# Kernel tuning notes

Measured on AMD Instinct MI355X. Metric: run time of the kernel, lower is better.

The kernel has to match this reference:

```python
import jax, jax.numpy as jnp
import numpy as np
from jax import lax

NUM_VARS = 16384
NUM_CHECKS = 8192
BATCH = 32
MAX_ITER = 15
H_DENSITY = 0.001  # ~8 ones per column, LDPC-like Tanner graph


def setup_inputs() -> dict:
    key = jax.random.key(0)
    k_h, k_s, k_l = jax.random.split(key, 3)
    # Sparse binary parity-check matrix represented densely (same math).
    parity_matrix = (jax.random.uniform(k_h, (NUM_CHECKS, NUM_VARS)) < H_DENSITY).astype(jnp.float32)
    syndrome = jax.random.randint(k_s, (BATCH, NUM_CHECKS), 0, 2).astype(jnp.float32)
    channel_llrs = jax.random.normal(k_l, (BATCH, NUM_VARS), dtype=jnp.float32)
    w_vc = jnp.ones((1,), dtype=jnp.float32)
    w_cv = jnp.ones((1,), dtype=jnp.float32)
    damping = jnp.float32(0.5)
    return {
        "syndrome": syndrome,
        "parity_matrix": parity_matrix,
        "channel_llrs": channel_llrs,
        "w_vc": w_vc,
        "w_cv": w_cv,
        "damping": damping,
    }


def reference(syndrome, parity_matrix, channel_llrs, w_vc, w_cv, damping):
    # syndrome: (B, C); parity_matrix H: (C, V); channel_llrs: (B, V)
    s_sign = 1.0 - 2.0 * syndrome  # (B, C)

    def body(v_beliefs, _):
        # v -> c: sparse.mm(H, v^T)^T == v @ H^T  -> (B, C)
        v_to_c = w_vc * (v_beliefs @ parity_matrix.T)
        c_msg = s_sign * jnp.tanh(v_to_c * 0.5)  # (B, C)
        # c -> v: sparse.mm(H^T, c^T)^T == c @ H  -> (B, V)
        c_to_v = w_cv * (c_msg @ parity_matrix)
        v_new = damping * v_beliefs + (1.0 - damping) * (channel_llrs + c_to_v)
        return v_new, None

    v_beliefs, _ = lax.scan(body, channel_llrs, None, length=MAX_ITER)
    return jax.nn.sigmoid(-v_beliefs)  # (B, V) bit-flip probabilities
```

## Files before the change

### kernel.cpp

```cpp
#include <hip/hip_runtime.h>


#define C_NUM 8192
#define V_NUM 16384
#define B_NUM 32
#define RW 64
#define CW 32

#define NBLK 256
#define NTHR 1024
#define NTH (NBLK * NTHR)

#define WCAP 256

typedef unsigned short u16;
typedef unsigned int u32;
typedef unsigned long long u64;

#define ZERO_WORDS ((C_NUM * 4 + V_NUM * 4 + C_NUM * RW * 2 + V_NUM * CW * 2) / 4)
#define NBAR 31
#define BAR_STRIDE 64

__device__ __forceinline__ float agent_ldf(const float* p) {
    return __hip_atomic_load(p, __ATOMIC_RELAXED, __HIP_MEMORY_SCOPE_AGENT);
}
__device__ __forceinline__ void agent_stf(float* p, float v) {
    __hip_atomic_store(p, v, __ATOMIC_RELAXED, __HIP_MEMORY_SCOPE_AGENT);
}
__device__ __forceinline__ u64 agent_ld64(const u64* p) {
    return __hip_atomic_load(p, __ATOMIC_RELAXED, __HIP_MEMORY_SCOPE_AGENT);
}
__device__ __forceinline__ int agent_ldi(const int* p) {
    return __hip_atomic_load(p, __ATOMIC_RELAXED, __HIP_MEMORY_SCOPE_AGENT);
}
__device__ __forceinline__ void agent_st32(u32* p, u32 v) {
    __hip_atomic_store(p, v, __ATOMIC_RELAXED, __HIP_MEMORY_SCOPE_AGENT);
}
__device__ __forceinline__ void agent_st16(u16* p, u16 v) {
    __hip_atomic_store(p, v, __ATOMIC_RELAXED, __HIP_MEMORY_SCOPE_AGENT);
}

__device__ __forceinline__ void grid_barrier(u32* bars, int id) {
    __syncthreads();
    if (threadIdx.x == 0) {
        u32* base = bars + id * 8 * BAR_STRIDE;
        asm volatile("s_waitcnt vmcnt(0) lgkmcnt(0)" ::: "memory");
        __hip_atomic_fetch_add(base + (blockIdx.x & 7) * BAR_STRIDE, 1u,
                               __ATOMIC_RELAXED, __HIP_MEMORY_SCOPE_AGENT);
        u32 sum;
        do {
            sum = 0;
#pragma unroll
            for (int g = 0; g < 8; ++g)
                sum += __hip_atomic_load(base + g * BAR_STRIDE,
                                         __ATOMIC_RELAXED, __HIP_MEMORY_SCOPE_AGENT);
            if (sum < (u32)NBLK) __builtin_amdgcn_s_sleep(4);
        } while (sum < (u32)NBLK);
        asm volatile("" ::: "memory");
    }
    __syncthreads();
}

__device__ __forceinline__ float fast_tanh_half(float x) {
    float ax = fabsf(x);
    float e = __expf(-ax);
    return copysignf((1.0f - e) / (1.0f + e), x);
}

__global__ __launch_bounds__(NTHR, 1)
void bp_fused(const float* __restrict__ H,
              const float* __restrict__ synd,
              const float* __restrict__ llr,
              const float* __restrict__ w_vc_p,
              const float* __restrict__ w_cv_p,
              const float* __restrict__ damp_p,
              int* __restrict__ row_cnt, int* __restrict__ col_cnt,
              u16* __restrict__ row_idx, u16* __restrict__ col_idx,
              float* __restrict__ bel, float* __restrict__ cms,
              u32* __restrict__ bars,
              float* __restrict__ out) {
    const int tid = blockIdx.x * NTHR + threadIdx.x;
    const int lane = threadIdx.x & 63;

    __shared__ u32 lds_edges[(NTHR / 64) * WCAP];
    u32* const wl = lds_edges + (threadIdx.x >> 6) * WCAP;

    {
        u32* zp = (u32*)row_cnt;
        for (int t = tid; t < ZERO_WORDS; t += NTH) agent_st32(&zp[t], 0u);
    }
    float llr_r[2], bel_r[2];
#pragma unroll
    for (int r = 0; r < 2; ++r) {
        int i = tid + r * NTH;
        int b = i & 31, v = i >> 5;
        float x = llr[b * V_NUM + v];
        llr_r[r] = x; bel_r[r] = x;
        agent_stf(&bel[i], x);
    }
    float ss_r;
    {
        int b = tid & 31, c = tid >> 5;
        ss_r = 1.0f - 2.0f * synd[b * C_NUM + c];
    }

    int wave_cnt;
    {
        const float4* Hv = (const float4*)H;
        const u64 ltmask = (1ull << lane) - 1ull;
        int wb = 0;
#pragma unroll 2
        for (int itn = 0; itn < 64; ++itn) {
            int t = tid + itn * (2 * NTH);
            float4 h0 = Hv[t];
            float4 h1 = Hv[t + NTH];
            float vals[8] = {h0.x, h0.y, h0.z, h0.w, h1.x, h1.y, h1.z, h1.w};
#pragma unroll
            for (int k = 0; k < 8; ++k) {
                bool nz = vals[k] != 0.0f;
                u64 b = __ballot(nz);
                if (b) {
                    if (nz) {
                        int ee = (k < 4) ? (t * 4 + k)
                                         : ((t + NTH) * 4 + (k - 4));
                        int off = wb + (int)__popcll(b & ltmask);
                        if (off < WCAP) wl[off] = (u32)ee;
                    }
                    wb += (int)__popcll(b);
                }
            }
        }
        wave_cnt = wb < WCAP ? wb : WCAP;
    }
    grid_barrier(bars, 0);

    {
        for (int e = lane; e < wave_cnt; e += 64) {
            u32 ee = wl[e];
            int c = (int)(ee >> 14);
            int v = (int)(ee & (V_NUM - 1));
            int rs = atomicAdd(&row_cnt[c], 1);
            if (rs < RW) agent_st16(&row_idx[c * RW + rs], (u16)v);
            int cs = atomicAdd(&col_cnt[v], 1);
            if (cs < CW) agent_st16(&col_idx[v * CW + cs], (u16)c);
        }
    }
    grid_barrier(bars, 1);

    int nrow_r;
    {
        int n = agent_ldi(&row_cnt[tid >> 5]);
        nrow_r = n > RW ? RW : n;
    }
    int ncol_r[2];
#pragma unroll
    for (int r = 0; r < 2; ++r) {
        int n = agent_ldi(&col_cnt[(tid + r * NTH) >> 5]);
        ncol_r[r] = n > CW ? CW : n;
    }
    const float wvc = w_vc_p[0];
    const float wcv = w_cv_p[0];
    const float d   = damp_p[0];

    int barid = 2;
    for (int it = 0; it < 15; ++it) {
        {
            int b = tid & 31, c = tid >> 5;
            int n = nrow_r;
            const u64* q4 = (const u64*)(row_idx + c * RW);
            float sum = 0.0f;
            int k4 = (n + 3) >> 2;
            for (int p = 0; p < k4; ++p) {
                u64 q = agent_ld64(&q4[p]);
                int j = 4 * p;
                int i0 = (int)(q & 0xFFFFu);
                int i1 = (int)((q >> 16) & 0xFFFFu);
                int i2 = (int)((q >> 32) & 0xFFFFu);
                int i3 = (int)(q >> 48);
                float s0 = agent_ldf(&bel[i0 * B_NUM + b]);
                float s1 = agent_ldf(&bel[i1 * B_NUM + b]);
                float s2 = agent_ldf(&bel[i2 * B_NUM + b]);
                float s3 = agent_ldf(&bel[i3 * B_NUM + b]);
                sum += s0;
                sum += (j + 1 < n) ? s1 : 0.0f;
                sum += (j + 2 < n) ? s2 : 0.0f;
                sum += (j + 3 < n) ? s3 : 0.0f;
            }
            agent_stf(&cms[tid], ss_r * fast_tanh_half(wvc * sum));
        }
        grid_barrier(bars, barid++);

        bool last = (it == 14);
#pragma unroll
        for (int r = 0; r < 2; ++r) {
            int i = tid + r * NTH;
            int b = i & 31, v = i >> 5;
            int n = ncol_r[r];
            const u64* q4 = (const u64*)(col_idx + v * CW);
            float sum = 0.0f;
            int k4 = (n + 3) >> 2;
            for (int p = 0; p < k4; ++p) {
                u64 q = agent_ld64(&q4[p]);
                int j = 4 * p;
                int i0 = (int)(q & 0xFFFFu);
                int i1 = (int)((q >> 16) & 0xFFFFu);
                int i2 = (int)((q >> 32) & 0xFFFFu);
                int i3 = (int)(q >> 48);
                float s0 = agent_ldf(&cms[i0 * B_NUM + b]);
                float s1 = agent_ldf(&cms[i1 * B_NUM + b]);
                float s2 = agent_ldf(&cms[i2 * B_NUM + b]);
                float s3 = agent_ldf(&cms[i3 * B_NUM + b]);
                sum += s0;
                sum += (j + 1 < n) ? s1 : 0.0f;
                sum += (j + 2 < n) ? s2 : 0.0f;
                sum += (j + 3 < n) ? s3 : 0.0f;
            }
            float nb = d * bel_r[r] + (1.0f - d) * (llr_r[r] + wcv * sum);
            bel_r[r] = nb;
            if (!last) {
                agent_stf(&bel[i], nb);
            } else {
                out[b * V_NUM + v] = 1.0f / (1.0f + __expf(nb));
            }
        }
        if (!last) grid_barrier(bars, barid++);
    }
}

extern "C" void kernel_launch(void* const* d_in, const int* in_sizes, int n_in,
                              void* d_out, int out_size, void* d_ws, size_t ws_size,
                              hipStream_t stream) {
    const float* synd = (const float*)d_in[0];
    const float* H    = (const float*)d_in[1];
    const float* llr  = (const float*)d_in[2];
    const float* w_vc = (const float*)d_in[3];
    const float* w_cv = (const float*)d_in[4];
    const float* damp = (const float*)d_in[5];
    float* out = (float*)d_out;

    char* ws = (char*)d_ws;
    size_t off = 0;
    int* row_cnt = (int*)(ws + off); off += (size_t)C_NUM * 4;
    int* col_cnt = (int*)(ws + off); off += (size_t)V_NUM * 4;
    u16* row_idx = (u16*)(ws + off); off += (size_t)C_NUM * RW * 2;
    u16* col_idx = (u16*)(ws + off); off += (size_t)V_NUM * CW * 2;
    float* bel = (float*)(ws + off); off += (size_t)V_NUM * B_NUM * 4;
    float* cms = (float*)(ws + off); off += (size_t)C_NUM * B_NUM * 4;
    u32* bars  = (u32*)(ws + off); off += (size_t)NBAR * 8 * BAR_STRIDE * 4;

    hipMemsetAsync(bars, 0, (size_t)NBAR * 8 * BAR_STRIDE * 4, stream);

    void* args[] = {
        (void*)&H, (void*)&synd, (void*)&llr,
        (void*)&w_vc, (void*)&w_cv, (void*)&damp,
        (void*)&row_cnt, (void*)&col_cnt, (void*)&row_idx, (void*)&col_idx,
        (void*)&bel, (void*)&cms, (void*)&bars, (void*)&out
    };
    hipLaunchCooperativeKernel((const void*)bp_fused,
                               dim3(NBLK), dim3(NTHR), args, 0, stream);
}
```

Before: 980.7 us.

## Cache row/column adjacency in registers, pad with zero sentinels, prefetch H scan

Before the iteration loop, each thread loads its check-node and variable-node neighbour index lists into registers (up to 48 row and 32 column entries). Unused slots point at a zeroed sentinel belief/message entry, so the per-element bounds selects go away. This removes the repeated index loads from global memory in each of the 15 iterations. The H compaction loop gains software prefetching of the next float4 pair. Risks are higher register pressure (launch bounds changed to 4) and silent truncation of rows with more than 48 nonzeros.

```diff
diff --git a/kernel.cpp b/kernel.cpp
--- a/kernel.cpp
+++ b/kernel.cpp
@@ -6,6 +6,9 @@
 #define B_NUM 32
 #define RW 64
 #define CW 32
+
+#define RQ 12
+#define CQ 8
 
 #define NBLK 256
 #define NTHR 1024
@@ -67,7 +70,7 @@
     return copysignf((1.0f - e) / (1.0f + e), x);
 }
 
-__global__ __launch_bounds__(NTHR, 1)
+__global__ __launch_bounds__(NTHR, 4)
 void bp_fused(const float* __restrict__ H,
               const float* __restrict__ synd,
               const float* __restrict__ llr,
@@ -88,6 +91,8 @@
     {
         u32* zp = (u32*)row_cnt;
         for (int t = tid; t < ZERO_WORDS; t += NTH) agent_st32(&zp[t], 0u);
+        if (tid < 32) agent_stf(&bel[V_NUM * B_NUM + tid], 0.0f);
+        else if (tid < 64) agent_stf(&cms[C_NUM * B_NUM + (tid - 32)], 0.0f);
     }
     float llr_r[2], bel_r[2];
 #pragma unroll
@@ -109,12 +114,15 @@
         const float4* Hv = (const float4*)H;
         const u64 ltmask = (1ull << lane) - 1ull;
         int wb = 0;
-#pragma unroll 2
+        int t = tid;
+        float4 c0 = Hv[t];
+        float4 c1 = Hv[t + NTH];
+#pragma unroll 1
         for (int itn = 0; itn < 64; ++itn) {
-            int t = tid + itn * (2 * NTH);
-            float4 h0 = Hv[t];
-            float4 h1 = Hv[t + NTH];
-            float vals[8] = {h0.x, h0.y, h0.z, h0.w, h1.x, h1.y, h1.z, h1.w};
+            float4 n0, n1;
+            int tn = t + 2 * NTH;
+            if (itn < 63) { n0 = Hv[tn]; n1 = Hv[tn + NTH]; }
+            float vals[8] = {c0.x, c0.y, c0.z, c0.w, c1.x, c1.y, c1.z, c1.w};
 #pragma unroll
             for (int k = 0; k < 8; ++k) {
                 bool nz = vals[k] != 0.0f;
@@ -129,6 +137,7 @@
                     wb += (int)__popcll(b);
                 }
             }
+            c0 = n0; c1 = n1; t = tn;
         }
         wave_cnt = wb < WCAP ? wb : WCAP;
     }
@@ -148,43 +157,64 @@
     grid_barrier(bars, 1);
 
     int nrow_r;
+    u64 rq[RQ];
     {
         int n = agent_ldi(&row_cnt[tid >> 5]);
-        nrow_r = n > RW ? RW : n;
+        nrow_r = n > 4 * RQ ? 4 * RQ : n;
+        const u64* q4 = (const u64*)(row_idx + (tid >> 5) * RW);
+#pragma unroll
+        for (int p = 0; p < RQ; ++p) {
+            u64 q = agent_ld64(&q4[p]);
+            int j = 4 * p;
+            u64 a0 = (j + 0 < nrow_r) ? (q & 0xFFFFu) : (u64)V_NUM;
+            u64 a1 = (j + 1 < nrow_r) ? ((q >> 16) & 0xFFFFu) : (u64)V_NUM;
+            u64 a2 = (j + 2 < nrow_r) ? ((q >> 32) & 0xFFFFu) : (u64)V_NUM;
+            u64 a3 = (j + 3 < nrow_r) ? (q >> 48) : (u64)V_NUM;
+            rq[p] = a0 | (a1 << 16) | (a2 << 32) | (a3 << 48);
+        }
     }
     int ncol_r[2];
+    u64 cq[2][CQ];
 #pragma unroll
     for (int r = 0; r < 2; ++r) {
-        int n = agent_ldi(&col_cnt[(tid + r * NTH) >> 5]);
-        ncol_r[r] = n > CW ? CW : n;
+        int v = (tid + r * NTH) >> 5;
+        int n = agent_ldi(&col_cnt[v]);
+        ncol_r[r] = n > 4 * CQ ? 4 * CQ : n;
+        const u64* q4 = (const u64*)(col_idx + v * CW);
+#pragma unroll
+        for (int p = 0; p < CQ; ++p) {
+            u64 q = agent_ld64(&q4[p]);
+            int j = 4 * p;
+            u64 a0 = (j + 0 < ncol_r[r]) ? (q & 0xFFFFu) : (u64)C_NUM;
+            u64 a1 = (j + 1 < ncol_r[r]) ? ((q >> 16) & 0xFFFFu) : (u64)C_NUM;
+            u64 a2 = (j + 2 < ncol_r[r]) ? ((q >> 32) & 0xFFFFu) : (u64)C_NUM;
+            u64 a3 = (j + 3 < ncol_r[r]) ? (q >> 48) : (u64)C_NUM;
+            cq[r][p] = a0 | (a1 << 16) | (a2 << 32) | (a3 << 48);
+        }
     }
     const float wvc = w_vc_p[0];
     const float wcv = w_cv_p[0];
     const float d   = damp_p[0];
 
+    const int b_lo = tid & 31;
     int barid = 2;
     for (int it = 0; it < 15; ++it) {
         {
-            int b = tid & 31, c = tid >> 5;
-            int n = nrow_r;
-            const u64* q4 = (const u64*)(row_idx + c * RW);
             float sum = 0.0f;
-            int k4 = (n + 3) >> 2;
-            for (int p = 0; p < k4; ++p) {
-                u64 q = agent_ld64(&q4[p]);
-                int j = 4 * p;
-                int i0 = (int)(q & 0xFFFFu);
-                int i1 = (int)((q >> 16) & 0xFFFFu);
-                int i2 = (int)((q >> 32) & 0xFFFFu);
-                int i3 = (int)(q >> 48);
-                float s0 = agent_ldf(&bel[i0 * B_NUM + b]);
-                float s1 = agent_ldf(&bel[i1 * B_NUM + b]);
-                float s2 = agent_ldf(&bel[i2 * B_NUM + b]);
-                float s3 = agent_ldf(&bel[i3 * B_NUM + b]);
-                sum += s0;
-                sum += (j + 1 < n) ? s1 : 0.0f;
-                sum += (j + 2 < n) ? s2 : 0.0f;
-                sum += (j + 3 < n) ? s3 : 0.0f;
+#pragma unroll
+            for (int p = 0; p < RQ; ++p) {
+                if (4 * p < nrow_r) {
+                    u64 q = rq[p];
+                    int i0 = (int)(q & 0xFFFFu);
+                    int i1 = (int)((q >> 16) & 0xFFFFu);
+                    int i2 = (int)((q >> 32) & 0xFFFFu);
+                    int i3 = (int)(q >> 48);
+                    float s0 = agent_ldf(&bel[i0 * B_NUM + b_lo]);
+                    float s1 = agent_ldf(&bel[i1 * B_NUM + b_lo]);
+                    float s2 = agent_ldf(&bel[i2 * B_NUM + b_lo]);
+                    float s3 = agent_ldf(&bel[i3 * B_NUM + b_lo]);
+                    sum += s0; sum += s1; sum += s2; sum += s3;
+                }
             }
             agent_stf(&cms[tid], ss_r * fast_tanh_half(wvc * sum));
         }
@@ -193,33 +223,29 @@
         bool last = (it == 14);
 #pragma unroll
         for (int r = 0; r < 2; ++r) {
-            int i = tid + r * NTH;
-            int b = i & 31, v = i >> 5;
-            int n = ncol_r[r];
-            const u64* q4 = (const u64*)(col_idx + v * CW);
             float sum = 0.0f;
-            int k4 = (n + 3) >> 2;
-            for (int p = 0; p < k4; ++p) {
-                u64 q = agent_ld64(&q4[p]);
-                int j = 4 * p;
-                int i0 = (int)(q & 0xFFFFu);
-                int i1 = (int)((q >> 16) & 0xFFFFu);
-                int i2 = (int)((q >> 32) & 0xFFFFu);
-                int i3 = (int)(q >> 48);
-                float s0 = agent_ldf(&cms[i0 * B_NUM + b]);
-                float s1 = agent_ldf(&cms[i1 * B_NUM + b]);
-                float s2 = agent_ldf(&cms[i2 * B_NUM + b]);
-                float s3 = agent_ldf(&cms[i3 * B_NUM + b]);
-                sum += s0;
-                sum += (j + 1 < n) ? s1 : 0.0f;
-                sum += (j + 2 < n) ? s2 : 0.0f;
-                sum += (j + 3 < n) ? s3 : 0.0f;
+#pragma unroll
+            for (int p = 0; p < CQ; ++p) {
+                if (4 * p < ncol_r[r]) {
+                    u64 q = cq[r][p];
+                    int i0 = (int)(q & 0xFFFFu);
+                    int i1 = (int)((q >> 16) & 0xFFFFu);
+                    int i2 = (int)((q >> 32) & 0xFFFFu);
+                    int i3 = (int)(q >> 48);
+                    float s0 = agent_ldf(&cms[i0 * B_NUM + b_lo]);
+                    float s1 = agent_ldf(&cms[i1 * B_NUM + b_lo]);
+                    float s2 = agent_ldf(&cms[i2 * B_NUM + b_lo]);
+                    float s3 = agent_ldf(&cms[i3 * B_NUM + b_lo]);
+                    sum += s0; sum += s1; sum += s2; sum += s3;
+                }
             }
             float nb = d * bel_r[r] + (1.0f - d) * (llr_r[r] + wcv * sum);
             bel_r[r] = nb;
+            int i = tid + r * NTH;
             if (!last) {
                 agent_stf(&bel[i], nb);
             } else {
+                int b = i & 31, v = i >> 5;
                 out[b * V_NUM + v] = 1.0f / (1.0f + __expf(nb));
             }
         }
@@ -244,8 +270,8 @@
     int* col_cnt = (int*)(ws + off); off += (size_t)V_NUM * 4;
     u16* row_idx = (u16*)(ws + off); off += (size_t)C_NUM * RW * 2;
     u16* col_idx = (u16*)(ws + off); off += (size_t)V_NUM * CW * 2;
-    float* bel = (float*)(ws + off); off += (size_t)V_NUM * B_NUM * 4;
-    float* cms = (float*)(ws + off); off += (size_t)C_NUM * B_NUM * 4;
+    float* bel = (float*)(ws + off); off += (size_t)V_NUM * B_NUM * 4 + 256;
+    float* cms = (float*)(ws + off); off += (size_t)C_NUM * B_NUM * 4 + 256;
     u32* bars  = (u32*)(ws + off); off += (size_t)NBAR * 8 * BAR_STRIDE * 4;
 
     hipMemsetAsync(bars, 0, (size_t)NBAR * 8 * BAR_STRIDE * 4, stream);
```

New measurement: 1.159 ms. +18.2%, slower.
